# Optimization experiments

Measured on AMD Instinct MI355X. Metric: run time of the kernel, lower is better.

Reference implementation:

```python
import jax, jax.numpy as jnp
import numpy as np

N_ITERATION = 3
NEG_INF = -1e18
EPS = 1e-8


def squash(t, eps=EPS):
    # t: [..., E]; scale = |t|^2/(1+|t|^2), out = scale * t / |t|
    sq = jnp.sum(t * t, axis=-1, keepdims=True)
    return (sq / (1.0 + sq)) * t / (jnp.sqrt(sq) + eps)


def setup_inputs() -> dict:
    key = jax.random.key(0)
    k1, k2, k3, k4 = jax.random.split(key, 4)
    B, K, L, D, O, E = 8, 1024, 1024, 1024, 6, 128
    inputs_u = jax.random.normal(k1, (B, K, D), dtype=jnp.float32)
    context_sequence = jax.random.normal(k2, (B, L, D), dtype=jnp.float32)
    # route_weights: [num_out_caps, d_model, d_per_capsule], fan-in scaled
    route_weights = jax.random.normal(k3, (O, D, E), dtype=jnp.float32) / np.sqrt(D)
    # True = padded in-capsule (masked)
    inputs_mask = jax.random.randint(k4, (B, K), 0, 2).astype(bool)
    return {
        "inputs_u": inputs_u,
        "context_sequence": context_sequence,
        "route_weights": route_weights,
        "inputs_mask": inputs_mask,
    }


def reference(inputs_u, context_sequence, route_weights, inputs_mask):
    # priors_u_hat: [B, K, O, E] (shared route weights across in-capsules)
    priors = jnp.einsum("bkd,ode->bkoe", inputs_u, route_weights)
    B, K, O, E = priors.shape
    L = context_sequence.shape[1]
    logits = jnp.zeros((B, L, K, O), dtype=priors.dtype)
    mask4 = inputs_mask[:, None, :, None]  # [B,1,K,1] -> broadcast to [B,L,K,O]
    outputs_v = None
    probs_c = None
    for i in range(N_ITERATION):
        lg = jnp.where(mask4, NEG_INF, logits)
        probs_c = jax.nn.softmax(lg, axis=-1)  # softmax over out-capsules
        # weighted aggregation over in-capsules then squash: [B,L,O,E]
        outputs_v = squash(jnp.einsum("blko,bkoe->bloe", probs_c, priors))
        if i != N_ITERATION - 1:
            # agreement delta logits: [B,L,K,O]
            logits = logits + jnp.einsum("bkoe,bloe->blko", priors, outputs_v)
    return outputs_v, probs_c
```

## Files before the change

kernel.cpp:

```cpp
#include <hip/hip_runtime.h>
#include <hip/hip_bf16.h>
#include <stdint.h>

typedef __bf16 bf16_t;
typedef __bf16 bf16x8 __attribute__((ext_vector_type(8)));
typedef float f32x4 __attribute__((ext_vector_type(4)));

#define BB 8
#define KK 1024
#define LL 1024
#define DD 1024
#define OO 6
#define EE 128
#define NN 768

__device__ __forceinline__ void async_copy16(const void* gptr, void* lds) {
    __builtin_amdgcn_global_load_lds(
        (__attribute__((address_space(1))) void*)gptr,
        (__attribute__((address_space(3))) void*)lds,
        16, 0, 0);
}

__device__ __forceinline__ void split_bf16(float x, bf16_t& hi, bf16_t& lo) {
    hi = (bf16_t)x;
    lo = (bf16_t)(x - (float)hi);
}

__global__ __launch_bounds__(256) void convert_a(
    const float* __restrict__ A, bf16_t* __restrict__ Ah, bf16_t* __restrict__ Al)
{
    const long i = ((long)blockIdx.x * 256 + threadIdx.x) * 4;
    const float4 x = *(const float4*)(A + i);
    union { bf16_t h[4]; uint2 u; } ph, pl;
    split_bf16(x.x, ph.h[0], pl.h[0]);
    split_bf16(x.y, ph.h[1], pl.h[1]);
    split_bf16(x.z, ph.h[2], pl.h[2]);
    split_bf16(x.w, ph.h[3], pl.h[3]);
    *(uint2*)(Ah + i) = ph.u;
    *(uint2*)(Al + i) = pl.u;
}

__global__ __launch_bounds__(256) void convert_w(
    const float* __restrict__ W, bf16_t* __restrict__ Wth, bf16_t* __restrict__ Wtl)
{
    __shared__ float t[32][33];
    const int o  = blockIdx.z;
    const int d0 = blockIdx.x * 32;
    const int e0 = blockIdx.y * 32;
    const int tx = threadIdx.x & 31;
    const int ty = threadIdx.x >> 5;
    const float* Wo = W + (long)o * DD * EE;
    bf16_t* Ho = Wth + (long)o * EE * DD;
    bf16_t* Lo = Wtl + (long)o * EE * DD;
#pragma unroll
    for (int p = 0; p < 4; ++p)
        t[p * 8 + ty][tx] = Wo[(long)(d0 + p * 8 + ty) * EE + e0 + tx];
    __syncthreads();
#pragma unroll
    for (int p = 0; p < 4; ++p) {
        const float val = t[tx][p * 8 + ty];
        bf16_t h, l;
        split_bf16(val, h, l);
        const long idx = (long)(e0 + p * 8 + ty) * DD + d0 + tx;
        Ho[idx] = h;
        Lo[idx] = l;
    }
}

__global__ __launch_bounds__(256) void gemm_priors(
    const bf16_t* __restrict__ Ah, const bf16_t* __restrict__ Al,
    const bf16_t* __restrict__ Bh, const bf16_t* __restrict__ Bl,
    float* __restrict__ C)
{
    __shared__ alignas(16) bf16_t sAh[128 * 32];
    __shared__ alignas(16) bf16_t sAl[128 * 32];
    __shared__ alignas(16) bf16_t sBh[128 * 32];
    __shared__ alignas(16) bf16_t sBl[128 * 32];

    const int tid  = threadIdx.x;
    const int w    = tid >> 6;
    const int lane = tid & 63;
    const int bm   = blockIdx.x;
    const int bn   = blockIdx.y;
    const int qr   = (w >> 1) * 64;
    const int qc   = (w & 1) * 64;
    const int r16  = lane & 15;
    const int q    = lane >> 4;

    f32x4 acc[4][4] = {};

    const int mrow = w * 32 + (lane >> 2);
    const int kcol = (lane & 3) * 8;

    const long aoff = (long)(bm * 128 + mrow) * DD + kcol;
    const long boff = (long)(bn * 128 + mrow) * DD + kcol;
    const bf16_t* gAh0 = Ah + aoff;  const bf16_t* gAh1 = gAh0 + 16 * DD;
    const bf16_t* gAl0 = Al + aoff;  const bf16_t* gAl1 = gAl0 + 16 * DD;
    const bf16_t* gBh0 = Bh + boff;  const bf16_t* gBh1 = gBh0 + 16 * DD;
    const bf16_t* gBl0 = Bl + boff;  const bf16_t* gBl1 = gBl0 + 16 * DD;

    bf16_t* lAh0 = sAh + (w * 2 + 0) * 512;  bf16_t* lAh1 = sAh + (w * 2 + 1) * 512;
    bf16_t* lAl0 = sAl + (w * 2 + 0) * 512;  bf16_t* lAl1 = sAl + (w * 2 + 1) * 512;
    bf16_t* lBh0 = sBh + (w * 2 + 0) * 512;  bf16_t* lBh1 = sBh + (w * 2 + 1) * 512;
    bf16_t* lBl0 = sBl + (w * 2 + 0) * 512;  bf16_t* lBl1 = sBl + (w * 2 + 1) * 512;

    for (int kt = 0; kt < DD / 32; ++kt) {
        const int k0 = kt * 32;
        async_copy16(gAh0 + k0, lAh0);
        async_copy16(gAh1 + k0, lAh1);
        async_copy16(gAl0 + k0, lAl0);
        async_copy16(gAl1 + k0, lAl1);
        async_copy16(gBh0 + k0, lBh0);
        async_copy16(gBh1 + k0, lBh1);
        async_copy16(gBl0 + k0, lBl0);
        async_copy16(gBl1 + k0, lBl1);
        __syncthreads();

        bf16x8 ah[4], al[4], bh[4], bl[4];
#pragma unroll
        for (int i = 0; i < 4; ++i) {
            const int ra = (qr + 16 * i + r16) * 32 + q * 8;
            ah[i] = *(const bf16x8*)(sAh + ra);
            al[i] = *(const bf16x8*)(sAl + ra);
        }
#pragma unroll
        for (int j = 0; j < 4; ++j) {
            const int rb = (qc + 16 * j + r16) * 32 + q * 8;
            bh[j] = *(const bf16x8*)(sBh + rb);
            bl[j] = *(const bf16x8*)(sBl + rb);
        }
#pragma unroll
        for (int i = 0; i < 4; ++i)
#pragma unroll
            for (int j = 0; j < 4; ++j) {
                acc[i][j] = __builtin_amdgcn_mfma_f32_16x16x32_bf16(
                    al[i], bh[j], acc[i][j], 0, 0, 0);
                acc[i][j] = __builtin_amdgcn_mfma_f32_16x16x32_bf16(
                    ah[i], bl[j], acc[i][j], 0, 0, 0);
                acc[i][j] = __builtin_amdgcn_mfma_f32_16x16x32_bf16(
                    ah[i], bh[j], acc[i][j], 0, 0, 0);
            }
        __syncthreads();
    }

#pragma unroll
    for (int i = 0; i < 4; ++i)
#pragma unroll
        for (int j = 0; j < 4; ++j) {
            const int col = bn * 128 + qc + 16 * j + r16;
#pragma unroll
            for (int r = 0; r < 4; ++r) {
                const int row = bm * 128 + qr + 16 * i + q * 4 + r;
                C[(long)row * NN + col] = acc[i][j][r];
            }
        }
}

__global__ __launch_bounds__(256) void probs_kernel(
    const float* __restrict__ g, const int* __restrict__ mask,
    float* __restrict__ probs)
{
    const int bk = blockIdx.x * 256 + threadIdx.x;
    if (bk >= BB * KK) return;
    if (mask[bk] != 0) {
        const float u = 1.0f / 6.0f;
#pragma unroll
        for (int o = 0; o < OO; ++o) probs[bk * OO + o] = u;
    } else {
        float p[OO];
        float m = -1e30f;
#pragma unroll
        for (int o = 0; o < OO; ++o) m = fmaxf(m, g[bk * OO + o]);
        float ssum = 0.f;
#pragma unroll
        for (int o = 0; o < OO; ++o) { p[o] = expf(g[bk * OO + o] - m); ssum += p[o]; }
        const float inv = 1.0f / ssum;
#pragma unroll
        for (int o = 0; o < OO; ++o) probs[bk * OO + o] = p[o] * inv;
    }
}

__global__ __launch_bounds__(256) void s_kernel(
    const float* __restrict__ priors, const float* __restrict__ probs,
    float* __restrict__ s)
{
    const int bo = blockIdx.x;
    const int b = bo / OO, o = bo % OO;
    const int kbase = blockIdx.y * 128;
    const int t = threadIdx.x;
    const int e = t & 127;
    const int kh = t >> 7;
    float accv = 0.f;
    const int k0 = kbase + kh * 64;
    for (int kk = 0; kk < 64; ++kk) {
        const long row = (long)(b * KK + k0 + kk) * OO + o;
        accv = fmaf(probs[row], priors[row * EE + e], accv);
    }
    __shared__ float red[256];
    red[t] = accv;
    __syncthreads();
    if (t < 128)
        atomicAdd(&s[b * NN + o * EE + e], red[t] + red[t + 128]);
}

__global__ __launch_bounds__(128) void squash_kernel(
    const float* __restrict__ s, float* __restrict__ v)
{
    const int bo = blockIdx.x;
    const int e = threadIdx.x;
    const float x = s[bo * EE + e];
    float sq = x * x;
#pragma unroll
    for (int off = 32; off > 0; off >>= 1) sq += __shfl_down(sq, off, 64);
    __shared__ float wsum[2];
    if ((threadIdx.x & 63) == 0) wsum[threadIdx.x >> 6] = sq;
    __syncthreads();
    const float total = wsum[0] + wsum[1];
    v[bo * EE + e] = total / (1.0f + total) * x / (sqrtf(total) + 1e-8f);
}

__global__ __launch_bounds__(256) void gupd_kernel(
    const float* __restrict__ priors, const float* __restrict__ v,
    float* __restrict__ g)
{
    const int wid = blockIdx.x * 4 + (threadIdx.x >> 6);
    const int lane = threadIdx.x & 63;
    const int b = wid / (KK * OO);
    const int o = wid % OO;
    const float* pr = priors + (long)wid * EE;
    const float* vb = v + b * NN + o * EE;
    float sum = pr[lane] * vb[lane] + pr[lane + 64] * vb[lane + 64];
#pragma unroll
    for (int off = 32; off > 0; off >>= 1) sum += __shfl_down(sum, off, 64);
    if (lane == 0) g[wid] += sum;
}

__global__ __launch_bounds__(256) void bcast_kernel(
    const float* __restrict__ V, const float* __restrict__ P,
    float* __restrict__ out)
{
    const long base = ((long)blockIdx.x * 256 + threadIdx.x) * 4;
    const long NV = (long)BB * LL * OO * EE;
    const float* src;
    if (base < NV) {
        const long b  = base / ((long)LL * OO * EE);
        const int off = (int)(base % NN);
        src = V + b * NN + off;
    } else {
        const long b2 = base - NV;
        const long b  = b2 / ((long)LL * KK * OO);
        const int off = (int)(b2 % (KK * OO));
        src = P + b * (KK * OO) + off;
    }
    *(float4*)(out + base) = *(const float4*)(src);
}

extern "C" void kernel_launch(void* const* d_in, const int* in_sizes, int n_in,
                              void* d_out, int out_size, void* d_ws, size_t ws_size,
                              hipStream_t stream)
{
    (void)in_sizes; (void)n_in; (void)out_size; (void)ws_size;
    const float* u    = (const float*)d_in[0];
    const float* W    = (const float*)d_in[2];
    const int*   mask = (const int*)d_in[3];
    float*       out  = (float*)d_out;

    char* ws = (char*)d_ws;
    size_t off = 0;
    float*  priors = (float*)(ws + off);  off += (size_t)8192 * NN * 4;
    bf16_t* Ah     = (bf16_t*)(ws + off); off += (size_t)8192 * DD * 2;
    bf16_t* Al     = (bf16_t*)(ws + off); off += (size_t)8192 * DD * 2;
    bf16_t* Wth    = (bf16_t*)(ws + off); off += (size_t)OO * EE * DD * 2;
    bf16_t* Wtl    = (bf16_t*)(ws + off); off += (size_t)OO * EE * DD * 2;
    float*  g      = (float*)(ws + off);  off += (size_t)BB * KK * OO * 4;
    float*  probs  = (float*)(ws + off);  off += (size_t)BB * KK * OO * 4;
    float*  s      = (float*)(ws + off);  off += (size_t)BB * NN * 4;
    float*  v      = (float*)(ws + off);

    hipLaunchKernelGGL(convert_a, dim3(8192), dim3(256), 0, stream, u, Ah, Al);
    hipLaunchKernelGGL(convert_w, dim3(32, 4, 6), dim3(256), 0, stream, W, Wth, Wtl);
    hipMemsetAsync(g, 0, BB * KK * OO * sizeof(float), stream);
    hipLaunchKernelGGL(gemm_priors, dim3(64, 6), dim3(256), 0, stream,
                       Ah, Al, Wth, Wtl, priors);

    for (int it = 0; it < 3; ++it) {
        hipLaunchKernelGGL(probs_kernel, dim3(32), dim3(256), 0, stream, g, mask, probs);
        hipMemsetAsync(s, 0, BB * NN * sizeof(float), stream);
        hipLaunchKernelGGL(s_kernel, dim3(48, 8), dim3(256), 0, stream, priors, probs, s);
        hipLaunchKernelGGL(squash_kernel, dim3(48), dim3(128), 0, stream, s, v);
        if (it < 2)
            hipLaunchKernelGGL(gupd_kernel, dim3(BB * KK * OO / 4), dim3(256), 0, stream,
                               priors, v, g);
    }
    hipLaunchKernelGGL(bcast_kernel, dim3(55296), dim3(256), 0, stream, v, probs, out);
}
```

Before: 387.9 us.

## Shrink GEMM N-tile, fuse logit update with softmax, drop atomics and memsets

Measured after the change: 372.7 us. -3.9%, faster.

```diff
diff --git a/kernel.cpp b/kernel.cpp
--- a/kernel.cpp
+++ b/kernel.cpp
@@ -74,8 +74,8 @@
 {
     __shared__ alignas(16) bf16_t sAh[128 * 32];
     __shared__ alignas(16) bf16_t sAl[128 * 32];
-    __shared__ alignas(16) bf16_t sBh[128 * 32];
-    __shared__ alignas(16) bf16_t sBl[128 * 32];
+    __shared__ alignas(16) bf16_t sBh[64 * 32];
+    __shared__ alignas(16) bf16_t sBl[64 * 32];
 
     const int tid  = threadIdx.x;
     const int w    = tid >> 6;
@@ -83,26 +83,29 @@
     const int bm   = blockIdx.x;
     const int bn   = blockIdx.y;
     const int qr   = (w >> 1) * 64;
-    const int qc   = (w & 1) * 64;
+    const int qc   = (w & 1) * 32;
     const int r16  = lane & 15;
     const int q    = lane >> 4;
 
-    f32x4 acc[4][4] = {};
-
-    const int mrow = w * 32 + (lane >> 2);
-    const int kcol = (lane & 3) * 8;
-
-    const long aoff = (long)(bm * 128 + mrow) * DD + kcol;
-    const long boff = (long)(bn * 128 + mrow) * DD + kcol;
+    f32x4 acc[4][2] = {};
+
+    const int mrowA = w * 32 + (lane >> 2);
+    const int mrowB = w * 16 + (lane >> 2);
+    const int kcol  = (lane & 3) * 8;
+
+    const long aoff = (long)(bm * 128 + mrowA) * DD + kcol;
+    const long boff = (long)(bn * 64  + mrowB) * DD + kcol;
     const bf16_t* gAh0 = Ah + aoff;  const bf16_t* gAh1 = gAh0 + 16 * DD;
     const bf16_t* gAl0 = Al + aoff;  const bf16_t* gAl1 = gAl0 + 16 * DD;
-    const bf16_t* gBh0 = Bh + boff;  const bf16_t* gBh1 = gBh0 + 16 * DD;
-    const bf16_t* gBl0 = Bl + boff;  const bf16_t* gBl1 = gBl0 + 16 * DD;
-
-    bf16_t* lAh0 = sAh + (w * 2 + 0) * 512;  bf16_t* lAh1 = sAh + (w * 2 + 1) * 512;
-    bf16_t* lAl0 = sAl + (w * 2 + 0) * 512;  bf16_t* lAl1 = sAl + (w * 2 + 1) * 512;
-    bf16_t* lBh0 = sBh + (w * 2 + 0) * 512;  bf16_t* lBh1 = sBh + (w * 2 + 1) * 512;
-    bf16_t* lBl0 = sBl + (w * 2 + 0) * 512;  bf16_t* lBl1 = sBl + (w * 2 + 1) * 512;
+    const bf16_t* gBh  = Bh + boff;
+    const bf16_t* gBl  = Bl + boff;
+
+    bf16_t* lAh0 = sAh + (w * 2 + 0) * 512;
+    bf16_t* lAh1 = sAh + (w * 2 + 1) * 512;
+    bf16_t* lAl0 = sAl + (w * 2 + 0) * 512;
+    bf16_t* lAl1 = sAl + (w * 2 + 1) * 512;
+    bf16_t* lBh  = sBh + w * 512;
+    bf16_t* lBl  = sBl + w * 512;
 
     for (int kt = 0; kt < DD / 32; ++kt) {
         const int k0 = kt * 32;
@@ -110,13 +113,11 @@
         async_copy16(gAh1 + k0, lAh1);
         async_copy16(gAl0 + k0, lAl0);
         async_copy16(gAl1 + k0, lAl1);
-        async_copy16(gBh0 + k0, lBh0);
-        async_copy16(gBh1 + k0, lBh1);
-        async_copy16(gBl0 + k0, lBl0);
-        async_copy16(gBl1 + k0, lBl1);
+        async_copy16(gBh  + k0, lBh);
+        async_copy16(gBl  + k0, lBl);
         __syncthreads();
 
-        bf16x8 ah[4], al[4], bh[4], bl[4];
+        bf16x8 ah[4], al[4], bh[2], bl[2];
 #pragma unroll
         for (int i = 0; i < 4; ++i) {
             const int ra = (qr + 16 * i + r16) * 32 + q * 8;
@@ -124,7 +125,7 @@
             al[i] = *(const bf16x8*)(sAl + ra);
         }
 #pragma unroll
-        for (int j = 0; j < 4; ++j) {
+        for (int j = 0; j < 2; ++j) {
             const int rb = (qc + 16 * j + r16) * 32 + q * 8;
             bh[j] = *(const bf16x8*)(sBh + rb);
             bl[j] = *(const bf16x8*)(sBl + rb);
@@ -132,7 +133,7 @@
 #pragma unroll
         for (int i = 0; i < 4; ++i)
 #pragma unroll
-            for (int j = 0; j < 4; ++j) {
+            for (int j = 0; j < 2; ++j) {
                 acc[i][j] = __builtin_amdgcn_mfma_f32_16x16x32_bf16(
                     al[i], bh[j], acc[i][j], 0, 0, 0);
                 acc[i][j] = __builtin_amdgcn_mfma_f32_16x16x32_bf16(
@@ -146,8 +147,8 @@
 #pragma unroll
     for (int i = 0; i < 4; ++i)
 #pragma unroll
-        for (int j = 0; j < 4; ++j) {
-            const int col = bn * 128 + qc + 16 * j + r16;
+        for (int j = 0; j < 2; ++j) {
+            const int col = bn * 64 + qc + 16 * j + r16;
 #pragma unroll
             for (int r = 0; r < 4; ++r) {
                 const int row = bm * 128 + qr + 16 * i + q * 4 + r;
@@ -156,33 +157,9 @@
         }
 }
 
-__global__ __launch_bounds__(256) void probs_kernel(
-    const float* __restrict__ g, const int* __restrict__ mask,
-    float* __restrict__ probs)
-{
-    const int bk = blockIdx.x * 256 + threadIdx.x;
-    if (bk >= BB * KK) return;
-    if (mask[bk] != 0) {
-        const float u = 1.0f / 6.0f;
-#pragma unroll
-        for (int o = 0; o < OO; ++o) probs[bk * OO + o] = u;
-    } else {
-        float p[OO];
-        float m = -1e30f;
-#pragma unroll
-        for (int o = 0; o < OO; ++o) m = fmaxf(m, g[bk * OO + o]);
-        float ssum = 0.f;
-#pragma unroll
-        for (int o = 0; o < OO; ++o) { p[o] = expf(g[bk * OO + o] - m); ssum += p[o]; }
-        const float inv = 1.0f / ssum;
-#pragma unroll
-        for (int o = 0; o < OO; ++o) probs[bk * OO + o] = p[o] * inv;
-    }
-}
-
 __global__ __launch_bounds__(256) void s_kernel(
     const float* __restrict__ priors, const float* __restrict__ probs,
-    float* __restrict__ s)
+    float* __restrict__ s_part, int uniform)
 {
     const int bo = blockIdx.x;
     const int b = bo / OO, o = bo % OO;
@@ -194,21 +171,24 @@
     const int k0 = kbase + kh * 64;
     for (int kk = 0; kk < 64; ++kk) {
         const long row = (long)(b * KK + k0 + kk) * OO + o;
-        accv = fmaf(probs[row], priors[row * EE + e], accv);
+        const float wgt = uniform ? (1.0f / 6.0f) : probs[row];
+        accv = fmaf(wgt, priors[row * EE + e], accv);
     }
     __shared__ float red[256];
     red[t] = accv;
     __syncthreads();
     if (t < 128)
-        atomicAdd(&s[b * NN + o * EE + e], red[t] + red[t + 128]);
+        s_part[((long)blockIdx.y * 48 + bo) * EE + e] = red[t] + red[t + 128];
 }
 
 __global__ __launch_bounds__(128) void squash_kernel(
-    const float* __restrict__ s, float* __restrict__ v)
+    const float* __restrict__ s_part, float* __restrict__ v)
 {
     const int bo = blockIdx.x;
     const int e = threadIdx.x;
-    const float x = s[bo * EE + e];
+    float x = 0.f;
+#pragma unroll
+    for (int y = 0; y < 8; ++y) x += s_part[((long)y * 48 + bo) * EE + e];
     float sq = x * x;
 #pragma unroll
     for (int off = 32; off > 0; off >>= 1) sq += __shfl_down(sq, off, 64);
@@ -219,20 +199,48 @@
     v[bo * EE + e] = total / (1.0f + total) * x / (sqrtf(total) + 1e-8f);
 }
 
-__global__ __launch_bounds__(256) void gupd_kernel(
+__global__ __launch_bounds__(256) void fused_pg_kernel(
     const float* __restrict__ priors, const float* __restrict__ v,
-    float* __restrict__ g)
-{
-    const int wid = blockIdx.x * 4 + (threadIdx.x >> 6);
+    const int* __restrict__ mask, float* __restrict__ g,
+    float* __restrict__ probs, int read_g, int store_g)
+{
+    const int wid  = blockIdx.x * 4 + (threadIdx.x >> 6);
     const int lane = threadIdx.x & 63;
-    const int b = wid / (KK * OO);
-    const int o = wid % OO;
-    const float* pr = priors + (long)wid * EE;
-    const float* vb = v + b * NN + o * EE;
-    float sum = pr[lane] * vb[lane] + pr[lane + 64] * vb[lane + 64];
-#pragma unroll
-    for (int off = 32; off > 0; off >>= 1) sum += __shfl_down(sum, off, 64);
-    if (lane == 0) g[wid] += sum;
+    const int b = wid >> 10;
+    const float* pr = priors + (long)wid * NN;
+    const float* vb = v + b * NN;
+
+    float po[OO];
+#pragma unroll
+    for (int o = 0; o < OO; ++o) {
+        const int j0 = o * EE + lane;
+        po[o] = pr[j0] * vb[j0] + pr[j0 + 64] * vb[j0 + 64];
+    }
+#pragma unroll
+    for (int off = 32; off > 0; off >>= 1)
+#pragma unroll
+        for (int o = 0; o < OO; ++o) po[o] += __shfl_xor(po[o], off, 64);
+
+    if (read_g) {
+#pragma unroll
+        for (int o = 0; o < OO; ++o) po[o] += g[wid * OO + o];
+    }
+    if (store_g && lane < OO) g[wid * OO + lane] = po[lane];
+
+    float p;
+    if (mask[wid] != 0) {
+        p = 1.0f / 6.0f;
+    } else {
+        float m = po[0];
+#pragma unroll
+        for (int o = 1; o < OO; ++o) m = fmaxf(m, po[o]);
+        float ssum = 0.f;
+#pragma unroll
+        for (int o = 0; o < OO; ++o) { po[o] = expf(po[o] - m); ssum += po[o]; }
+        const float inv = 1.0f / ssum;
+        p = ((lane < OO) ? po[lane] : 0.f) * inv;
+    }
+    if (lane < OO) probs[wid * OO + lane] = p;
 }
 
 __global__ __launch_bounds__(256) void bcast_kernel(
@@ -274,23 +282,29 @@
     bf16_t* Wtl    = (bf16_t*)(ws + off); off += (size_t)OO * EE * DD * 2;
     float*  g      = (float*)(ws + off);  off += (size_t)BB * KK * OO * 4;
     float*  probs  = (float*)(ws + off);  off += (size_t)BB * KK * OO * 4;
-    float*  s      = (float*)(ws + off);  off += (size_t)BB * NN * 4;
+    float*  s_part = (float*)(ws + off);  off += (size_t)8 * 48 * EE * 4;
     float*  v      = (float*)(ws + off);
 
     hipLaunchKernelGGL(convert_a, dim3(8192), dim3(256), 0, stream, u, Ah, Al);
     hipLaunchKernelGGL(convert_w, dim3(32, 4, 6), dim3(256), 0, stream, W, Wth, Wtl);
-    hipMemsetAsync(g, 0, BB * KK * OO * sizeof(float), stream);
-    hipLaunchKernelGGL(gemm_priors, dim3(64, 6), dim3(256), 0, stream,
+    hipLaunchKernelGGL(gemm_priors, dim3(64, 12), dim3(256), 0, stream,
                        Ah, Al, Wth, Wtl, priors);
 
-    for (int it = 0; it < 3; ++it) {
-        hipLaunchKernelGGL(probs_kernel, dim3(32), dim3(256), 0, stream, g, mask, probs);
-        hipMemsetAsync(s, 0, BB * NN * sizeof(float), stream);
-        hipLaunchKernelGGL(s_kernel, dim3(48, 8), dim3(256), 0, stream, priors, probs, s);
-        hipLaunchKernelGGL(squash_kernel, dim3(48), dim3(128), 0, stream, s, v);
-        if (it < 2)
-            hipLaunchKernelGGL(gupd_kernel, dim3(BB * KK * OO / 4), dim3(256), 0, stream,
-                               priors, v, g);
-    }
+    hipLaunchKernelGGL(s_kernel, dim3(48, 8), dim3(256), 0, stream,
+                       priors, (const float*)nullptr, s_part, 1);
+    hipLaunchKernelGGL(squash_kernel, dim3(48), dim3(128), 0, stream, s_part, v);
+
+    hipLaunchKernelGGL(fused_pg_kernel, dim3(2048), dim3(256), 0, stream,
+                       priors, v, mask, g, probs, 0, 1);
+    hipLaunchKernelGGL(s_kernel, dim3(48, 8), dim3(256), 0, stream,
+                       priors, probs, s_part, 0);
+    hipLaunchKernelGGL(squash_kernel, dim3(48), dim3(128), 0, stream, s_part, v);
+
+    hipLaunchKernelGGL(fused_pg_kernel, dim3(2048), dim3(256), 0, stream,
+                       priors, v, mask, g, probs, 1, 0);
+    hipLaunchKernelGGL(s_kernel, dim3(48, 8), dim3(256), 0, stream,
+                       priors, probs, s_part, 0);
+    hipLaunchKernelGGL(squash_kernel, dim3(48), dim3(128), 0, stream, s_part, v);
+
     hipLaunchKernelGGL(bcast_kernel, dim3(55296), dim3(256), 0, stream, v, probs, out);
 }
```
